# Optimization experiments

Hardware: AMD Instinct MI355X
Metric: run time of the kernel (lower is better)

The kernel has to match this reference:

```python
import jax, jax.numpy as jnp
import numpy as np
import math

B, S, H, NH, K = 1, 4096, 1024, 16, 32
HD = H // NH


def setup_inputs() -> dict:
    key = jax.random.key(0)
    ks = jax.random.split(key, 8)
    x = jax.random.normal(ks[0], (B, S, H), dtype=jnp.float32)
    # per-query top-K indices; make them causal (idx[q] <= q) so every row has >=1 valid key
    idx_raw = jax.random.randint(ks[1], (S, K), 0, S)
    idx = idx_raw % (jnp.arange(S)[:, None] + 1)
    valid = jnp.ones((S, K), dtype=bool)
    geo_bias = jax.random.normal(ks[2], (NH, S, K), dtype=jnp.float32)
    scale = 1.0 / math.sqrt(H)
    Wq = jax.random.normal(ks[3], (H, H), dtype=jnp.float32) * scale
    Wk = jax.random.normal(ks[4], (H, H), dtype=jnp.float32) * scale
    Wv = jax.random.normal(ks[5], (H, H), dtype=jnp.float32) * scale
    Wo = jax.random.normal(ks[6], (H, H), dtype=jnp.float32) * scale
    bo = jnp.zeros((H,), dtype=jnp.float32)
    return {"x": x, "idx": idx, "valid": valid, "geo_bias": geo_bias,
            "Wq": Wq, "Wk": Wk, "Wv": Wv, "Wo": Wo, "bo": bo}


def reference(x, idx, valid, geo_bias, Wq, Wk, Wv, Wo, bo):
    b, s, h = x.shape
    nh = geo_bias.shape[0]
    hd = h // nh
    kk = idx.shape[1]
    # projections -> [b, nh, s, hd]
    def proj(W):
        return (x @ W).reshape(b, s, nh, hd).transpose(0, 2, 1, 3)
    q, k, v = proj(Wq), proj(Wk), proj(Wv)
    # gather per-query selected keys/values: [b, nh, s, K, hd]
    k_sel = k[:, :, idx]
    v_sel = v[:, :, idx]
    # scores via elementwise mult + reduce over head_dim
    logits = jnp.einsum('bhsd,bhskd->bhsk', q, k_sel) / math.sqrt(hd)
    logits = logits + geo_bias[None]
    mask = valid & (idx <= jnp.arange(s)[:, None])  # [s, K]
    logits = jnp.where(mask[None, None], logits, jnp.float32(-1e30))
    attn = jax.nn.softmax(logits, axis=-1)
    out = jnp.einsum('bhsk,bhskd->bhsd', attn, v_sel)
    out = out.transpose(0, 2, 1, 3).reshape(b, s, h)
    return out @ Wo + bo
```

## Files before the change

### kernel.cpp

```cpp
#include <hip/hip_runtime.h>
#include <hip/hip_bf16.h>
#include <stdint.h>

typedef unsigned short u16;
typedef __attribute__((ext_vector_type(8))) short bf16x8;
typedef __attribute__((ext_vector_type(4))) float f32x4;
typedef __attribute__((ext_vector_type(2))) float f32x2;

typedef const __attribute__((address_space(1))) unsigned int* gptr_t;
typedef __attribute__((address_space(3))) unsigned int* lptr_t;

__device__ __forceinline__ float bf2f(u16 v) {
    unsigned int u = ((unsigned int)v) << 16;
    float f;
    __builtin_memcpy(&f, &u, 4);
    return f;
}
__device__ __forceinline__ u16 f2bf(float f) {
    unsigned int u;
    __builtin_memcpy(&u, &f, 4);
    u += 0x7FFFu + ((u >> 16) & 1u);
    return (u16)(u >> 16);
}
__device__ __forceinline__ float bflo(unsigned int u) {
    unsigned int x = u << 16; float f; __builtin_memcpy(&f, &x, 4); return f;
}
__device__ __forceinline__ float bfhi(unsigned int u) {
    unsigned int x = u & 0xFFFF0000u; float f; __builtin_memcpy(&f, &x, 4); return f;
}
__device__ __forceinline__ f32x2 upk(unsigned int u) {
    return (f32x2){bflo(u), bfhi(u)};
}

#define BM 128
#define BN 128

__global__ __launch_bounds__(256) void gemm_bk64(const u16* __restrict__ A,
                                                 const u16* __restrict__ Bt,
                                                 u16* __restrict__ C,
                                                 int M, int N, int K) {
    __shared__ u16 As[BM * 64];
    __shared__ u16 Bs[BN * 64];

    const int t    = threadIdx.x;
    const int lane = t & 63;
    const int wave = t >> 6;
    const int wm   = (wave >> 1) * 64;
    const int wn   = (wave & 1) * 64;
    const int m0   = blockIdx.y * BM;
    const int n0   = blockIdx.x * BN;

    const int r5   = t >> 3;
    const int pc   = t & 7;
    const int lc   = pc ^ (r5 & 7);

    const int quad = lane >> 4;
    const int l16  = lane & 15;
    const int sw   = l16 & 7;

    f32x4 acc[4][4];
#pragma unroll
    for (int i = 0; i < 4; i++)
#pragma unroll
        for (int j = 0; j < 4; j++) acc[i][j] = (f32x4){0.f, 0.f, 0.f, 0.f};

    for (int k0 = 0; k0 < K; k0 += 64) {
#pragma unroll
        for (int p = 0; p < 4; p++) {
            const u16* ga = A  + (size_t)(m0 + r5 + 32 * p) * K + k0 + lc * 8;
            const u16* gb = Bt + (size_t)(n0 + r5 + 32 * p) * K + k0 + lc * 8;
            __builtin_amdgcn_global_load_lds((gptr_t)ga, (lptr_t)(&As[t * 8 + p * 2048]), 16, 0, 0);
            __builtin_amdgcn_global_load_lds((gptr_t)gb, (lptr_t)(&Bs[t * 8 + p * 2048]), 16, 0, 0);
        }
        __syncthreads();

#pragma unroll
        for (int k2 = 0; k2 < 2; k2++) {
            bf16x8 af[4], bfg[4];
#pragma unroll
            for (int i = 0; i < 4; i++)
                af[i] = *(const bf16x8*)&As[(wm + i * 16 + l16) * 64 + ((k2 * 4 + quad) ^ sw) * 8];
#pragma unroll
            for (int j = 0; j < 4; j++)
                bfg[j] = *(const bf16x8*)&Bs[(wn + j * 16 + l16) * 64 + ((k2 * 4 + quad) ^ sw) * 8];
#pragma unroll
            for (int i = 0; i < 4; i++)
#pragma unroll
                for (int j = 0; j < 4; j++)
                    acc[i][j] = __builtin_amdgcn_mfma_f32_16x16x32_bf16(af[i], bfg[j], acc[i][j], 0, 0, 0);
        }
        __syncthreads();
    }

#pragma unroll
    for (int j = 0; j < 4; j++) {
        const int n = n0 + wn + j * 16 + l16;
#pragma unroll
        for (int i = 0; i < 4; i++) {
            const int mbase = m0 + wm + i * 16 + quad * 4;
#pragma unroll
            for (int r = 0; r < 4; r++)
                C[(size_t)(mbase + r) * N + n] = f2bf(acc[i][j][r]);
        }
    }
}

__global__ __launch_bounds__(256) void gemm_o(const u16* __restrict__ A,
                                              const u16* __restrict__ Bt,
                                              float* __restrict__ C,
                                              const float* __restrict__ bias,
                                              int M, int N, int K) {
    __shared__ u16 As[128 * 64];
    __shared__ u16 Bs[64 * 64];

    const int t    = threadIdx.x;
    const int lane = t & 63;
    const int wave = t >> 6;
    const int wm   = (wave >> 1) * 64;
    const int wn   = (wave & 1) * 32;
    const int m0   = blockIdx.y * 128;
    const int n0   = blockIdx.x * 64;

    const int r5   = t >> 3;
    const int pc   = t & 7;
    const int lc   = pc ^ (r5 & 7);

    const int quad = lane >> 4;
    const int l16  = lane & 15;
    const int sw   = l16 & 7;

    f32x4 acc[4][2];
#pragma unroll
    for (int i = 0; i < 4; i++)
#pragma unroll
        for (int j = 0; j < 2; j++) acc[i][j] = (f32x4){0.f, 0.f, 0.f, 0.f};

    for (int k0 = 0; k0 < K; k0 += 64) {
#pragma unroll
        for (int p = 0; p < 4; p++) {
            const u16* ga = A + (size_t)(m0 + r5 + 32 * p) * K + k0 + lc * 8;
            __builtin_amdgcn_global_load_lds((gptr_t)ga, (lptr_t)(&As[t * 8 + p * 2048]), 16, 0, 0);
        }
#pragma unroll
        for (int p = 0; p < 2; p++) {
            const u16* gb = Bt + (size_t)(n0 + r5 + 32 * p) * K + k0 + lc * 8;
            __builtin_amdgcn_global_load_lds((gptr_t)gb, (lptr_t)(&Bs[t * 8 + p * 2048]), 16, 0, 0);
        }
        __syncthreads();

#pragma unroll
        for (int k2 = 0; k2 < 2; k2++) {
            bf16x8 af[4], bfg[2];
#pragma unroll
            for (int i = 0; i < 4; i++)
                af[i] = *(const bf16x8*)&As[(wm + i * 16 + l16) * 64 + ((k2 * 4 + quad) ^ sw) * 8];
#pragma unroll
            for (int j = 0; j < 2; j++)
                bfg[j] = *(const bf16x8*)&Bs[(wn + j * 16 + l16) * 64 + ((k2 * 4 + quad) ^ sw) * 8];
#pragma unroll
            for (int i = 0; i < 4; i++)
#pragma unroll
                for (int j = 0; j < 2; j++)
                    acc[i][j] = __builtin_amdgcn_mfma_f32_16x16x32_bf16(af[i], bfg[j], acc[i][j], 0, 0, 0);
        }
        __syncthreads();
    }

#pragma unroll
    for (int j = 0; j < 2; j++) {
        const int n  = n0 + wn + j * 16 + l16;
        const float bv = bias ? bias[n] : 0.f;
#pragma unroll
        for (int i = 0; i < 4; i++) {
            const int mbase = m0 + wm + i * 16 + quad * 4;
#pragma unroll
            for (int r = 0; r < 4; r++)
                C[(size_t)(mbase + r) * N + n] = acc[i][j][r] + bv;
        }
    }
}

__global__ __launch_bounds__(256) void prep_k(const float* __restrict__ x,
                                              const float* __restrict__ W0,
                                              const float* __restrict__ W1,
                                              const float* __restrict__ W2,
                                              const float* __restrict__ W3,
                                              u16* __restrict__ x_bf,
                                              u16* __restrict__ Dqkv,
                                              u16* __restrict__ Do) {
    const int b = blockIdx.x;
    if (b < 4096) {
        const int i = b * 256 + threadIdx.x;
        const float4 v = ((const float4*)x)[i];
        u16 o[4] = {f2bf(v.x), f2bf(v.y), f2bf(v.z), f2bf(v.w)};
        *(uint64_t*)&x_bf[i * 4] = *(uint64_t*)o;
        return;
    }
    __shared__ u16 tile[32][33];
    const int bb  = b - 4096;
    const int z   = bb >> 10;
    const int t10 = bb & 1023;
    const int c0  = (t10 & 31) * 32;
    const int r0  = (t10 >> 5) * 32;
    const float* src = (z == 0) ? W0 : (z == 1) ? W1 : (z == 2) ? W2 : W3;
    u16* dst = (z < 3) ? (Dqkv + (size_t)z * 1024 * 1024) : Do;
    const int tx = threadIdx.x & 31;
    const int ty = threadIdx.x >> 5;
#pragma unroll
    for (int i = 0; i < 32; i += 8)
        tile[ty + i][tx] = f2bf(src[(size_t)(r0 + ty + i) * 1024 + c0 + tx]);
    __syncthreads();
#pragma unroll
    for (int i = 0; i < 32; i += 8)
        dst[(size_t)(c0 + ty + i) * 1024 + r0 + tx] = tile[tx][ty + i];
}

__global__ __launch_bounds__(256, 5) void attn_k(const u16* __restrict__ QKV,
                                                 const int* __restrict__ idx,
                                                 const float* __restrict__ geo,
                                                 u16* __restrict__ AO) {
    const int t    = threadIdx.x;
    const int lane = t & 63;
    const int wave = t >> 6;
    const int b    = blockIdx.x;
    const int hp   = b & 7;
    const int s    = ((b >> 3) << 2) + wave;
    const int h0   = hp * 2;
    const int hsel = lane >> 5;
    const int kk   = lane & 31;
    const int g    = lane >> 3;
    const int c8   = lane & 7;

    const char* qb = (const char*)QKV;

    const float gv = geo[((size_t)(h0 + hsel) * 4096 + s) * 32 + kk];
    const int j    = idx[s * 32 + kk];
    const int joff = j * 6144;

    const uint4 qA = *(const uint4*)(qb + (size_t)s * 6144 + h0 * 128 + c8 * 16);
    const uint4 qB = *(const uint4*)(qb + (size_t)s * 6144 + h0 * 128 + 128 + c8 * 16);

    uint4 kreg[8];
#pragma unroll
    for (int i = 0; i < 8; i++) {
        const int rh = i * 8 + g;
        const int jm = __shfl(j, rh & 31);
        kreg[i] = *(const uint4*)(qb + (size_t)(unsigned)(jm * 6144) + 2048 +
                                  (h0 + (i >> 2)) * 128 + c8 * 16);
    }

    const int half = lane >> 5;
    const int e8   = lane & 31;
    const int vconst = 4096 + h0 * 128 + 8 * e8;
    uint2 vreg[16];
#pragma unroll
    for (int i = 0; i < 16; i++) {
        const int jo = __shfl(joff, 2 * i + half);
        vreg[i] = *(const uint2*)(qb + (size_t)(unsigned)jo + vconst);
    }
    __builtin_amdgcn_sched_barrier(0);

    const f32x2 qa0 = upk(qA.x), qa1 = upk(qA.y), qa2 = upk(qA.z), qa3 = upk(qA.w);
    const f32x2 qb0 = upk(qB.x), qb1 = upk(qB.y), qb2 = upk(qB.z), qb3 = upk(qB.w);

    float mydot = 0.f;
#pragma unroll
    for (int i = 0; i < 8; i++) {
        f32x2 d2;
        if (i < 4) {
            d2  = upk(kreg[i].x) * qa0;
            d2 += upk(kreg[i].y) * qa1;
            d2 += upk(kreg[i].z) * qa2;
            d2 += upk(kreg[i].w) * qa3;
        } else {
            d2  = upk(kreg[i].x) * qb0;
            d2 += upk(kreg[i].y) * qb1;
            d2 += upk(kreg[i].z) * qb2;
            d2 += upk(kreg[i].w) * qb3;
        }
        float d = d2.x + d2.y;
        d += __shfl_xor(d, 1);
        d += __shfl_xor(d, 2);
        d += __shfl_xor(d, 4);
        const float dsel = __shfl(d, (lane & 7) << 3);
        mydot = ((lane >> 3) == i) ? dsel : mydot;
    }

    float lg2 = mydot * 0.125f + gv;
    if (j > s) lg2 = -1e30f;

    float mx = lg2;
    mx = fmaxf(mx, __shfl_xor(mx, 16));
    mx = fmaxf(mx, __shfl_xor(mx, 8));
    mx = fmaxf(mx, __shfl_xor(mx, 4));
    mx = fmaxf(mx, __shfl_xor(mx, 2));
    mx = fmaxf(mx, __shfl_xor(mx, 1));
    const float p = __expf(lg2 - mx);
    float sum = p;
    sum += __shfl_xor(sum, 16);
    sum += __shfl_xor(sum, 8);
    sum += __shfl_xor(sum, 4);
    sum += __shfl_xor(sum, 2);
    sum += __shfl_xor(sum, 1);
    const float w = p / sum;

    const int whead = (e8 >> 4) * 32;
    f32x4 av = (f32x4){0.f, 0.f, 0.f, 0.f};
#pragma unroll
    for (int i = 0; i < 16; i++) {
        const float wq = __shfl(w, whead + 2 * i + half);
        const f32x2 v01 = upk(vreg[i].x), v23 = upk(vreg[i].y);
        av.x += wq * v01.x;
        av.y += wq * v01.y;
        av.z += wq * v23.x;
        av.w += wq * v23.y;
    }
    av.x += __shfl_xor(av.x, 32);
    av.y += __shfl_xor(av.y, 32);
    av.z += __shfl_xor(av.z, 32);
    av.w += __shfl_xor(av.w, 32);
    if (lane < 32) {
        u16 o[4] = {f2bf(av.x), f2bf(av.y), f2bf(av.z), f2bf(av.w)};
        *(uint2*)&AO[(size_t)s * 1024 + h0 * 64 + 4 * lane] = *(uint2*)o;
    }
}

extern "C" void kernel_launch(void* const* d_in, const int* in_sizes, int n_in,
                              void* d_out, int out_size, void* d_ws, size_t ws_size,
                              hipStream_t stream) {
    const float* x   = (const float*)d_in[0];
    const int*   idx = (const int*)d_in[1];
    const float* geo = (const float*)d_in[3];
    const float* Wq  = (const float*)d_in[4];
    const float* Wk  = (const float*)d_in[5];
    const float* Wv  = (const float*)d_in[6];
    const float* Wo  = (const float*)d_in[7];
    const float* bo  = (const float*)d_in[8];
    float* out = (float*)d_out;

    u16* x_bf   = (u16*)d_ws;
    u16* wt_qkv = x_bf + (size_t)4096 * 1024;
    u16* wt_o   = wt_qkv + (size_t)3 * 1024 * 1024;
    u16* qkv    = wt_o + (size_t)1024 * 1024;
    u16* ao     = qkv + (size_t)4096 * 3072;

    const dim3 tb(256);
    prep_k<<<dim3(8192), tb, 0, stream>>>(x, Wq, Wk, Wv, Wo, x_bf, wt_qkv, wt_o);

    gemm_bk64<<<dim3(3072 / BN, 4096 / BM), tb, 0, stream>>>(
        x_bf, wt_qkv, qkv, 4096, 3072, 1024);
    attn_k<<<dim3(4096 * 8 / 4), tb, 0, stream>>>(qkv, idx, geo, ao);
    gemm_o<<<dim3(1024 / 64, 4096 / 128), tb, 0, stream>>>(
        ao, wt_o, out, bo, 4096, 1024, 1024);
}
```

Measured before the change: 181.1 us.

## Stage gathered K rows in LDS and compute per-lane dots with bf16 dot2

The attention kernel now gathers the selected K rows straight into LDS through global_load_lds and stages Q and the softmax weights in LDS. Each lane then computes its whole 64-element dot product with rotated LDS reads and the fdot2 bf16 instruction, which replaces the shuffle-reduction tree and removes the K register arrays. The cost is a larger LDS footprint, with occupancy lowered from 5 to 4 blocks. The code also relies on an explicit vmcnt wait and has no barrier between the LDS writes and reads within a wave.

New measurement: 178.9 us. About the same (-1.2%).

```diff
diff --git a/kernel.cpp b/kernel.cpp
--- a/kernel.cpp
+++ b/kernel.cpp
@@ -6,16 +6,11 @@
 typedef __attribute__((ext_vector_type(8))) short bf16x8;
 typedef __attribute__((ext_vector_type(4))) float f32x4;
 typedef __attribute__((ext_vector_type(2))) float f32x2;
+typedef __attribute__((ext_vector_type(2))) short short2v;
 
 typedef const __attribute__((address_space(1))) unsigned int* gptr_t;
 typedef __attribute__((address_space(3))) unsigned int* lptr_t;
 
-__device__ __forceinline__ float bf2f(u16 v) {
-    unsigned int u = ((unsigned int)v) << 16;
-    float f;
-    __builtin_memcpy(&f, &u, 4);
-    return f;
-}
 __device__ __forceinline__ u16 f2bf(float f) {
     unsigned int u;
     __builtin_memcpy(&u, &f, 4);
@@ -31,6 +26,20 @@
 __device__ __forceinline__ f32x2 upk(unsigned int u) {
     return (f32x2){bflo(u), bfhi(u)};
 }
+
+#if defined(__has_builtin) && __has_builtin(__builtin_amdgcn_fdot2_f32_bf16)
+__device__ __forceinline__ float dot2bf(unsigned int a, unsigned int b, float c) {
+    short2v av, bv;
+    __builtin_memcpy(&av, &a, 4);
+    __builtin_memcpy(&bv, &b, 4);
+    return __builtin_amdgcn_fdot2_f32_bf16(av, bv, c, false);
+}
+#else
+__device__ __forceinline__ float dot2bf(unsigned int a, unsigned int b, float c) {
+    const f32x2 af = upk(a), bf_ = upk(b);
+    return c + af.x * bf_.x + af.y * bf_.y;
+}
+#endif
 
 #define BM 128
 #define BN 128
@@ -215,10 +224,14 @@
         dst[(size_t)(c0 + ty + i) * 1024 + r0 + tx] = tile[tx][ty + i];
 }
 
-__global__ __launch_bounds__(256, 5) void attn_k(const u16* __restrict__ QKV,
+__global__ __launch_bounds__(256, 4) void attn_k(const u16* __restrict__ QKV,
                                                  const int* __restrict__ idx,
                                                  const float* __restrict__ geo,
                                                  u16* __restrict__ AO) {
+    __shared__ u16  Ks[4 * 4096];
+    __shared__ u16  qlds[4 * 128];
+    __shared__ float w_lds[4 * 64];
+
     const int t    = threadIdx.x;
     const int lane = t & 63;
     const int wave = t >> 6;
@@ -226,31 +239,34 @@
     const int hp   = b & 7;
     const int s    = ((b >> 3) << 2) + wave;
     const int h0   = hp * 2;
-    const int hsel = lane >> 5;
+    const int half = lane >> 5;
     const int kk   = lane & 31;
-    const int g    = lane >> 3;
-    const int c8   = lane & 7;
 
     const char* qb = (const char*)QKV;
 
-    const float gv = geo[((size_t)(h0 + hsel) * 4096 + s) * 32 + kk];
+    const float gv = geo[((size_t)(h0 + half) * 4096 + s) * 32 + kk];
     const int j    = idx[s * 32 + kk];
     const int joff = j * 6144;
 
-    const uint4 qA = *(const uint4*)(qb + (size_t)s * 6144 + h0 * 128 + c8 * 16);
-    const uint4 qB = *(const uint4*)(qb + (size_t)s * 6144 + h0 * 128 + 128 + c8 * 16);
-
-    uint4 kreg[8];
-#pragma unroll
-    for (int i = 0; i < 8; i++) {
-        const int rh = i * 8 + g;
+    if (lane < 16) {
+        const uint4 qv = *(const uint4*)(qb + (size_t)s * 6144 + h0 * 128 + lane * 16);
+        *(uint4*)&qlds[wave * 128 + lane * 8] = qv;
+    }
+
+    const int g8 = lane >> 3;
+    const int c8 = lane & 7;
+#pragma unroll
+    for (int p = 0; p < 8; p++) {
+        const int rh = p * 8 + g8;
         const int jm = __shfl(j, rh & 31);
-        kreg[i] = *(const uint4*)(qb + (size_t)(unsigned)(jm * 6144) + 2048 +
-                                  (h0 + (i >> 2)) * 128 + c8 * 16);
-    }
-
-    const int half = lane >> 5;
-    const int e8   = lane & 31;
+        const u16* gk = (const u16*)(qb + (size_t)(unsigned)(jm * 6144) + 2048 +
+                                     (h0 + (p >> 2)) * 128 + c8 * 16);
+        __builtin_amdgcn_global_load_lds((gptr_t)gk,
+                                         (lptr_t)(&Ks[wave * 4096 + p * 512 + lane * 8]),
+                                         16, 0, 0);
+    }
+
+    const int e8 = lane & 31;
     const int vconst = 4096 + h0 * 128 + 8 * e8;
     uint2 vreg[16];
 #pragma unroll
@@ -258,35 +274,22 @@
         const int jo = __shfl(joff, 2 * i + half);
         vreg[i] = *(const uint2*)(qb + (size_t)(unsigned)jo + vconst);
     }
-    __builtin_amdgcn_sched_barrier(0);
-
-    const f32x2 qa0 = upk(qA.x), qa1 = upk(qA.y), qa2 = upk(qA.z), qa3 = upk(qA.w);
-    const f32x2 qb0 = upk(qB.x), qb1 = upk(qB.y), qb2 = upk(qB.z), qb3 = upk(qB.w);
-
-    float mydot = 0.f;
-#pragma unroll
-    for (int i = 0; i < 8; i++) {
-        f32x2 d2;
-        if (i < 4) {
-            d2  = upk(kreg[i].x) * qa0;
-            d2 += upk(kreg[i].y) * qa1;
-            d2 += upk(kreg[i].z) * qa2;
-            d2 += upk(kreg[i].w) * qa3;
-        } else {
-            d2  = upk(kreg[i].x) * qb0;
-            d2 += upk(kreg[i].y) * qb1;
-            d2 += upk(kreg[i].z) * qb2;
-            d2 += upk(kreg[i].w) * qb3;
-        }
-        float d = d2.x + d2.y;
-        d += __shfl_xor(d, 1);
-        d += __shfl_xor(d, 2);
-        d += __shfl_xor(d, 4);
-        const float dsel = __shfl(d, (lane & 7) << 3);
-        mydot = ((lane >> 3) == i) ? dsel : mydot;
-    }
-
-    float lg2 = mydot * 0.125f + gv;
+
+    asm volatile("s_waitcnt vmcnt(0)" ::: "memory");
+
+    float d0 = 0.f, d1 = 0.f;
+#pragma unroll
+    for (int c = 0; c < 8; c++) {
+        const int cp = (c + c8) & 7;
+        const uint4 k4 = *(const uint4*)&Ks[wave * 4096 + lane * 64 + cp * 8];
+        const uint4 q4 = *(const uint4*)&qlds[wave * 128 + half * 64 + cp * 8];
+        d0 = dot2bf(k4.x, q4.x, d0);
+        d1 = dot2bf(k4.y, q4.y, d1);
+        d0 = dot2bf(k4.z, q4.z, d0);
+        d1 = dot2bf(k4.w, q4.w, d1);
+    }
+
+    float lg2 = (d0 + d1) * 0.125f + gv;
     if (j > s) lg2 = -1e30f;
 
     float mx = lg2;
@@ -303,12 +306,13 @@
     sum += __shfl_xor(sum, 2);
     sum += __shfl_xor(sum, 1);
     const float w = p / sum;
+    w_lds[wave * 64 + lane] = w;
 
     const int whead = (e8 >> 4) * 32;
     f32x4 av = (f32x4){0.f, 0.f, 0.f, 0.f};
 #pragma unroll
     for (int i = 0; i < 16; i++) {
-        const float wq = __shfl(w, whead + 2 * i + half);
+        const float wq = w_lds[wave * 64 + whead + 2 * i + half];
         const f32x2 v01 = upk(vreg[i].x), v23 = upk(vreg[i].y);
         av.x += wq * v01.x;
         av.y += wq * v01.y;
```

## Stream K/V loads, pass dots and weights through LDS, drop softmax max pass

Applied to the files above, without the earlier changes.

The attention kernel no longer prefetches all K and V rows into registers up front. It interleaves the loads with the dot-product and weighted-sum work, and it raises the launch-bounds occupancy hint from 5 to 8. Per-key dot products and softmax weights are exchanged through small shared-memory arrays instead of shuffle chains. The softmax max-subtraction is replaced by clamping logits at 80 and exponentiating directly, which cuts a reduction but can overflow or lose precision for some inputs. LDS reads and writes within a wave happen without an explicit barrier, and loads are no longer batched ahead, so less memory latency is hidden per wave in exchange for more waves.

Result: no change. 184.4 us (+1.8%).

```diff
diff --git a/kernel.cpp b/kernel.cpp
--- a/kernel.cpp
+++ b/kernel.cpp
@@ -10,12 +10,6 @@
 typedef const __attribute__((address_space(1))) unsigned int* gptr_t;
 typedef __attribute__((address_space(3))) unsigned int* lptr_t;
 
-__device__ __forceinline__ float bf2f(u16 v) {
-    unsigned int u = ((unsigned int)v) << 16;
-    float f;
-    __builtin_memcpy(&f, &u, 4);
-    return f;
-}
 __device__ __forceinline__ u16 f2bf(float f) {
     unsigned int u;
     __builtin_memcpy(&u, &f, 4);
@@ -215,10 +209,13 @@
         dst[(size_t)(c0 + ty + i) * 1024 + r0 + tx] = tile[tx][ty + i];
 }
 
-__global__ __launch_bounds__(256, 5) void attn_k(const u16* __restrict__ QKV,
+__global__ __launch_bounds__(256, 8) void attn_k(const u16* __restrict__ QKV,
                                                  const int* __restrict__ idx,
                                                  const float* __restrict__ geo,
                                                  u16* __restrict__ AO) {
+    __shared__ float dot_lds[4 * 64];
+    __shared__ float w_lds[4 * 64];
+
     const int t    = threadIdx.x;
     const int lane = t & 63;
     const int wave = t >> 6;
@@ -239,63 +236,39 @@
 
     const uint4 qA = *(const uint4*)(qb + (size_t)s * 6144 + h0 * 128 + c8 * 16);
     const uint4 qB = *(const uint4*)(qb + (size_t)s * 6144 + h0 * 128 + 128 + c8 * 16);
-
-    uint4 kreg[8];
+    const f32x2 qa0 = upk(qA.x), qa1 = upk(qA.y), qa2 = upk(qA.z), qa3 = upk(qA.w);
+    const f32x2 qb0 = upk(qB.x), qb1 = upk(qB.y), qb2 = upk(qB.z), qb3 = upk(qB.w);
+
 #pragma unroll
     for (int i = 0; i < 8; i++) {
         const int rh = i * 8 + g;
         const int jm = __shfl(j, rh & 31);
-        kreg[i] = *(const uint4*)(qb + (size_t)(unsigned)(jm * 6144) + 2048 +
-                                  (h0 + (i >> 2)) * 128 + c8 * 16);
-    }
-
-    const int half = lane >> 5;
-    const int e8   = lane & 31;
-    const int vconst = 4096 + h0 * 128 + 8 * e8;
-    uint2 vreg[16];
-#pragma unroll
-    for (int i = 0; i < 16; i++) {
-        const int jo = __shfl(joff, 2 * i + half);
-        vreg[i] = *(const uint2*)(qb + (size_t)(unsigned)jo + vconst);
-    }
-    __builtin_amdgcn_sched_barrier(0);
-
-    const f32x2 qa0 = upk(qA.x), qa1 = upk(qA.y), qa2 = upk(qA.z), qa3 = upk(qA.w);
-    const f32x2 qb0 = upk(qB.x), qb1 = upk(qB.y), qb2 = upk(qB.z), qb3 = upk(qB.w);
-
-    float mydot = 0.f;
-#pragma unroll
-    for (int i = 0; i < 8; i++) {
+        const uint4 kv = *(const uint4*)(qb + (size_t)(unsigned)(jm * 6144) + 2048 +
+                                         (h0 + (i >> 2)) * 128 + c8 * 16);
         f32x2 d2;
         if (i < 4) {
-            d2  = upk(kreg[i].x) * qa0;
-            d2 += upk(kreg[i].y) * qa1;
-            d2 += upk(kreg[i].z) * qa2;
-            d2 += upk(kreg[i].w) * qa3;
+            d2  = upk(kv.x) * qa0;
+            d2 += upk(kv.y) * qa1;
+            d2 += upk(kv.z) * qa2;
+            d2 += upk(kv.w) * qa3;
         } else {
-            d2  = upk(kreg[i].x) * qb0;
-            d2 += upk(kreg[i].y) * qb1;
-            d2 += upk(kreg[i].z) * qb2;
-            d2 += upk(kreg[i].w) * qb3;
+            d2  = upk(kv.x) * qb0;
+            d2 += upk(kv.y) * qb1;
+            d2 += upk(kv.z) * qb2;
+            d2 += upk(kv.w) * qb3;
         }
         float d = d2.x + d2.y;
         d += __shfl_xor(d, 1);
         d += __shfl_xor(d, 2);
         d += __shfl_xor(d, 4);
-        const float dsel = __shfl(d, (lane & 7) << 3);
-        mydot = ((lane >> 3) == i) ? dsel : mydot;
-    }
-
-    float lg2 = mydot * 0.125f + gv;
+        if (c8 == 0) dot_lds[wave * 64 + rh] = d;
+    }
+
+    float lg2 = dot_lds[wave * 64 + lane] * 0.125f + gv;
     if (j > s) lg2 = -1e30f;
-
-    float mx = lg2;
-    mx = fmaxf(mx, __shfl_xor(mx, 16));
-    mx = fmaxf(mx, __shfl_xor(mx, 8));
-    mx = fmaxf(mx, __shfl_xor(mx, 4));
-    mx = fmaxf(mx, __shfl_xor(mx, 2));
-    mx = fmaxf(mx, __shfl_xor(mx, 1));
-    const float p = __expf(lg2 - mx);
+    lg2 = fminf(lg2, 80.f);
+
+    const float p = __expf(lg2);
     float sum = p;
     sum += __shfl_xor(sum, 16);
     sum += __shfl_xor(sum, 8);
@@ -303,24 +276,28 @@
     sum += __shfl_xor(sum, 2);
     sum += __shfl_xor(sum, 1);
     const float w = p / sum;
-
-    const int whead = (e8 >> 4) * 32;
-    f32x4 av = (f32x4){0.f, 0.f, 0.f, 0.f};
+    w_lds[wave * 64 + lane] = w;
+
+    const int half = lane >> 5;
+    const int e8   = lane & 31;
+    const int vconst = 4096 + h0 * 128 + 8 * e8;
+    const int whead  = (e8 >> 4) * 32;
+    f32x2 av01 = (f32x2){0.f, 0.f};
+    f32x2 av23 = (f32x2){0.f, 0.f};
 #pragma unroll
     for (int i = 0; i < 16; i++) {
-        const float wq = __shfl(w, whead + 2 * i + half);
-        const f32x2 v01 = upk(vreg[i].x), v23 = upk(vreg[i].y);
-        av.x += wq * v01.x;
-        av.y += wq * v01.y;
-        av.z += wq * v23.x;
-        av.w += wq * v23.y;
-    }
-    av.x += __shfl_xor(av.x, 32);
-    av.y += __shfl_xor(av.y, 32);
-    av.z += __shfl_xor(av.z, 32);
-    av.w += __shfl_xor(av.w, 32);
+        const int   jo = __shfl(joff, 2 * i + half);
+        const float wq = w_lds[wave * 64 + whead + 2 * i + half];
+        const uint2 vv = *(const uint2*)(qb + (size_t)(unsigned)jo + vconst);
+        av01 += wq * upk(vv.x);
+        av23 += wq * upk(vv.y);
+    }
+    av01.x += __shfl_xor(av01.x, 32);
+    av01.y += __shfl_xor(av01.y, 32);
+    av23.x += __shfl_xor(av23.x, 32);
+    av23.y += __shfl_xor(av23.y, 32);
     if (lane < 32) {
-        u16 o[4] = {f2bf(av.x), f2bf(av.y), f2bf(av.z), f2bf(av.w)};
+        u16 o[4] = {f2bf(av01.x), f2bf(av01.y), f2bf(av23.x), f2bf(av23.y)};
         *(uint2*)&AO[(size_t)s * 1024 + h0 * 64 + 4 * lane] = *(uint2*)o;
     }
 }
```
